# Optimization experiments

Measured on AMD Instinct MI355X. Metric: run time of the kernel, lower is better.

## Reference

```python
import math
import jax, jax.numpy as jnp
import numpy as np

HID_DIM = 1024
N_HEAD = 16
HEAD_DIM = HID_DIM // N_HEAD
NEG_FILL = -1e9


def _alibi_slopes(n_head: int) -> np.ndarray:
    """ALiBi per-head slopes (Press et al. 2021), matching get_slopes()."""
    main = 2 ** int(math.log2(n_head))
    m = (2.0 ** (-8.0 / main)) ** np.arange(1, 1 + main)
    if main < n_head:
        intra = (2.0 ** (-4.0 / main)) ** np.arange(1, 1 + 2 * (n_head - main), 2)
        m = np.concatenate([m, intra])
    return m.astype(np.float32)  # [H]


def setup_inputs() -> dict:
    key = jax.random.key(0)
    k1, k2, k3 = jax.random.split(key, 3)
    B, S = 2, 2048
    x = jax.random.normal(k1, (B, S, HID_DIM), dtype=jnp.float32)
    mask = jnp.ones((B, S), dtype=jnp.int32)
    Wqkv = jax.random.normal(k2, (HID_DIM, 3 * HID_DIM), dtype=jnp.float32) * 0.02
    Wout = jax.random.normal(k3, (HID_DIM, HID_DIM), dtype=jnp.float32) * 0.02
    return {"x": x, "mask": mask, "Wqkv": Wqkv, "Wout": Wout}


def reference(x, mask, Wqkv, Wout):
    B, S, _ = x.shape
    qkv = x @ Wqkv  # [B,S,3*hid]
    q, k, v = jnp.split(qkv, 3, axis=-1)
    k_cache, v_cache = k, v  # current_cache (pre-reshape, [B,S,hid])

    def to_heads(t):
        return t.reshape(B, S, N_HEAD, HEAD_DIM).transpose(0, 2, 1, 3)  # [B,H,S,Dh]

    q, k, v = to_heads(q), to_heads(k), to_heads(v)

    # NOTE: original code computes self.dk but never scales QK^T by it.
    scores = jnp.einsum('bhqd,bhkd->bhqk', q, k)  # [B,H,S,S]

    # ALiBi bias: tril(j - i), zero on/above diagonal elsewhere per torch.tril
    pos = jnp.arange(S)
    alibi = jnp.tril(pos[None, :] - pos[:, None]).astype(scores.dtype)  # [S,S]
    slopes = jnp.asarray(_alibi_slopes(N_HEAD))  # [H]
    scores = scores + slopes[None, :, None, None] * alibi[None, None]

    # padding mask broadcast over key dim: mask[:,None,None,:]
    scores = jnp.where(mask[:, None, None, :] == 0, NEG_FILL, scores)

    probs = jax.nn.softmax(scores, axis=-1)
    attn = jnp.einsum('bhqk,bhkd->bhqd', probs, v)  # [B,H,S,Dh]
    attn = attn.transpose(0, 2, 1, 3).reshape(B, S, HID_DIM)
    out = attn @ Wout  # dropout is identity in eval / p=0
    return out, k_cache, v_cache
```

## Files before the change

### kernel.cpp

```cpp
#include <hip/hip_runtime.h>
#include <hip/hip_bf16.h>
#include <cstdint>
#include <cstddef>

#define HID 1024
#define NH 16
#define DH 64
#define SEQ 2048
#define BATCH 2
#define BS (BATCH*SEQ)
#define LOG2E 1.4426950408889634f
#define PAD 68

typedef __attribute__((ext_vector_type(8))) short bf16x8;
typedef __attribute__((ext_vector_type(4))) float f32x4;

static __device__ __forceinline__ float fast_exp2(float x) {
    return __builtin_amdgcn_exp2f(x);
}

static __device__ __forceinline__ short f2bf(float f) {
    union { __hip_bfloat16 h; short s; } cv;
    cv.h = __float2bfloat16(f);
    return cv.s;
}
static __device__ __forceinline__ unsigned pack2(float a, float b) {
    union { __hip_bfloat162 h2; unsigned u; } cv;
    cv.h2 = __float22bfloat162_rn(make_float2(a, b));
    return cv.u;
}

typedef const __attribute__((address_space(1))) unsigned gas_u32;
typedef __attribute__((address_space(3))) unsigned las_u32;
static __device__ __forceinline__ void gload_lds16(const short* g, short* l) {
    __builtin_amdgcn_global_load_lds((gas_u32*)g, (las_u32*)l, 16, 0, 0);
}

__global__ __launch_bounds__(256)
void prep(const float* __restrict__ Wqkv, const float* __restrict__ Wout,
          const float* __restrict__ x,
          short* __restrict__ wqkvT, short* __restrict__ woutT,
          short* __restrict__ xb)
{
    __shared__ short tl[64][66];
    const int bid = blockIdx.x;
    const int t = threadIdx.x;

    if (bid >= 1024) {
        const float4* x4 = (const float4*)x;
        uint2* xo = (uint2*)xb;
        const int base = (bid - 1024) * 4096 + t;
        #pragma unroll
        for (int i = 0; i < 16; ++i) {
            float4 f = x4[base + i*256];
            xo[base + i*256] = make_uint2(pack2(f.x, f.y), pack2(f.z, f.w));
        }
        return;
    }

    const float* W; short* WT; int Nw, K, k0, n0;
    if (bid < 768) {
        W = Wqkv; WT = wqkvT; Nw = 3072; K = 1024;
        n0 = (bid % 48) * 64; k0 = (bid / 48) * 64;
    } else {
        W = Wout; WT = woutT; Nw = 1024; K = 1024;
        int b2 = bid - 768;
        n0 = (b2 & 15) * 64; k0 = (b2 >> 4) * 64;
    }
    const int r = t >> 2, c0 = (t & 3) * 16;
    const float* src = W + (size_t)(k0 + r) * Nw + n0 + c0;
    #pragma unroll
    for (int i = 0; i < 16; i += 4) {
        float4 f = *(const float4*)(src + i);
        tl[r][c0+i+0] = f2bf(f.x); tl[r][c0+i+1] = f2bf(f.y);
        tl[r][c0+i+2] = f2bf(f.z); tl[r][c0+i+3] = f2bf(f.w);
    }
    __syncthreads();
    short* dst = WT + (size_t)(n0 + r) * K + k0 + c0;
    unsigned buf[8];
    #pragma unroll
    for (int i = 0; i < 8; ++i) {
        unsigned lo = (unsigned short)tl[c0 + 2*i    ][r];
        unsigned hi = (unsigned short)tl[c0 + 2*i + 1][r];
        buf[i] = lo | (hi << 16);
    }
    *(uint4*)dst       = *(uint4*)&buf[0];
    *((uint4*)dst + 1) = *(uint4*)&buf[4];
}

template<int CMODE, int BN>
__global__ __launch_bounds__(256, 3)
void gemm_lds(const short* __restrict__ A, const short* __restrict__ Bt,
              float* __restrict__ Cf,
              float* __restrict__ kc, float* __restrict__ vc,
              short* __restrict__ qb, short* __restrict__ kb, short* __restrict__ vt,
              int M, int N, int K)
{
    constexpr int WN = BN / 2;
    constexpr int NF = WN / 16;
    __shared__ short As[128*64];
    __shared__ short Bs[BN*64];
    const int t    = threadIdx.x;
    const int wave = t >> 6, lane = t & 63;
    const int quad = lane >> 4, l16 = lane & 15;
    const int wrow = (wave & 1) * 64, wcol = (wave >> 1) * WN;
    const int n0 = blockIdx.x * BN, m0 = blockIdx.y * 128;

    f32x4 acc[4][NF];
    #pragma unroll
    for (int mi = 0; mi < 4; ++mi)
        #pragma unroll
        for (int nj = 0; nj < NF; ++nj) acc[mi][nj] = (f32x4){0.f,0.f,0.f,0.f};

    const int lr = lane >> 3;
    const int lc = (lane & 7) * 8;
    const short* Ab = A  + (size_t)(m0 + wave*32       + lr) * K + lc;
    const short* Bb = Bt + (size_t)(n0 + wave*(BN/4)   + lr) * K + lc;
    short* AsW = As + (wave*32)      * 64;
    short* BsW = Bs + (wave*(BN/4))  * 64;

    for (int kt = 0; kt < K; kt += 64) {
        #pragma unroll
        for (int i = 0; i < 4; ++i)
            gload_lds16(Ab + (size_t)(i*8)*K + kt, AsW + i*512);
        #pragma unroll
        for (int i = 0; i < BN/32; ++i)
            gload_lds16(Bb + (size_t)(i*8)*K + kt, BsW + i*512);
        __syncthreads();

        #pragma unroll
        for (int ks = 0; ks < 2; ++ks) {
            bf16x8 af[4], bfr[NF];
            #pragma unroll
            for (int mi = 0; mi < 4; ++mi)
                af[mi] = *(const bf16x8*)&As[(wrow + mi*16 + l16)*64 + ks*32 + quad*8];
            #pragma unroll
            for (int nj = 0; nj < NF; ++nj)
                bfr[nj] = *(const bf16x8*)&Bs[(wcol + nj*16 + l16)*64 + ks*32 + quad*8];
            #pragma unroll
            for (int mi = 0; mi < 4; ++mi)
                #pragma unroll
                for (int nj = 0; nj < NF; ++nj)
                    acc[mi][nj] = __builtin_amdgcn_mfma_f32_16x16x32_bf16(
                        af[mi], bfr[nj], acc[mi][nj], 0, 0, 0);
        }
        __syncthreads();
    }

    const int region = (CMODE == 0) ? (n0 >> 10) : 0;
    #pragma unroll
    for (int mi = 0; mi < 4; ++mi) {
        int rbase = m0 + wrow + mi*16 + quad*4;
        #pragma unroll
        for (int nj = 0; nj < NF; ++nj) {
            int col = n0 + wcol + nj*16 + l16;
            if (CMODE == 1) {
                #pragma unroll
                for (int reg = 0; reg < 4; ++reg)
                    Cf[(size_t)(rbase + reg) * N + col] = acc[mi][nj][reg];
            } else {
                int c = col & 1023;
                if (region == 0) {
                    #pragma unroll
                    for (int reg = 0; reg < 4; ++reg)
                        qb[(size_t)(rbase + reg) * HID + c] = f2bf(acc[mi][nj][reg] * LOG2E);
                } else if (region == 1) {
                    #pragma unroll
                    for (int reg = 0; reg < 4; ++reg) {
                        float v = acc[mi][nj][reg];
                        kc[(size_t)(rbase + reg) * HID + c] = v;
                        if (kb) kb[(size_t)(rbase + reg) * HID + c] = f2bf(v);
                    }
                } else {
                    #pragma unroll
                    for (int reg = 0; reg < 4; ++reg)
                        vc[(size_t)(rbase + reg) * HID + c] = acc[mi][nj][reg];
                    if (vt) {
                        int b = rbase >> 11, s = rbase & 2047;
                        int h = c >> 6, d = c & 63;
                        unsigned u[2] = {pack2(acc[mi][nj][0], acc[mi][nj][1]),
                                         pack2(acc[mi][nj][2], acc[mi][nj][3])};
                        *(uint2*)&vt[((size_t)((b*16 + h)*64 + d)) * SEQ + s] = *(uint2*)u;
                    }
                }
            }
        }
    }
}

template<bool KVB>
__global__ __launch_bounds__(256, 4)
void attn_kernel(const short* qb,
                 const short* __restrict__ kb, const short* __restrict__ vtg,
                 const float* __restrict__ kc, const float* __restrict__ vc,
                 const int*   __restrict__ mask,
                 short* attn_b)
{
    __shared__ short Ks[64*PAD];
    __shared__ short Vs[64*PAD];
    __shared__ short Ps[64*PAD];
    __shared__ float Mk[64];

    const int t    = threadIdx.x;
    const int wave = t >> 6, lane = t & 63;
    const int quad = lane >> 4, l16 = lane & 15;

    const int blk = blockIdx.x;
    const int qt  = blk & 31;
    const int h   = (blk >> 5) & 15;
    const int b   = blk >> 9;
    const int q0  = qt * 64;
    const float slope2 = exp2f(-0.5f * (float)(h + 1)) * LOG2E;
    const int* mb = mask + b * SEQ;

    const int r  = t >> 2;
    const int c0 = (t & 3) * 16;

    const int qrow0 = q0 + 16*wave + quad*4;

    bf16x8 aq[2];
    #pragma unroll
    for (int ks = 0; ks < 2; ++ks)
        aq[ks] = *(const bf16x8*)(qb + ((size_t)(b*SEQ + q0 + 16*wave + l16)) * HID
                                     + h*DH + ks*32 + quad*8);

    float ls[4];
    f32x4 Oacc[4];
    #pragma unroll
    for (int i = 0; i < 4; ++i) {
        ls[i] = 0.f;
        Oacc[i] = (f32x4){0.f,0.f,0.f,0.f};
    }

    if (KVB) {
        uint4 kr0, kr1, vr0, vr1; float mval = 0.f;
        const short* kbase = kb  + ((size_t)(b*SEQ + r)) * HID + h*DH + c0;
        const short* vbase = vtg + ((size_t)((b*NH + h)*DH + r)) * SEQ + c0;

        kr0 = *(const uint4*)(kbase);
        kr1 = *(const uint4*)(kbase + 8);
        vr0 = *(const uint4*)(vbase);
        vr1 = *(const uint4*)(vbase + 8);
        if (t < 64) mval = (mb[t] == 0) ? -2.0e9f : 0.f;

        for (int kt = 0; kt < 32; ++kt) {
            const int j0 = kt * 64;
            __syncthreads();

            *(uint4*)&Ks[r*PAD + c0]     = kr0;
            *(uint4*)&Ks[r*PAD + c0 + 8] = kr1;
            *(uint4*)&Vs[r*PAD + c0]     = vr0;
            *(uint4*)&Vs[r*PAD + c0 + 8] = vr1;
            if (t < 64) Mk[t] = mval;

            if (kt < 31) {
                const short* kn = kbase + (size_t)(j0 + 64) * HID;
                const short* vn = vbase + (j0 + 64);
                kr0 = *(const uint4*)(kn);
                kr1 = *(const uint4*)(kn + 8);
                vr0 = *(const uint4*)(vn);
                vr1 = *(const uint4*)(vn + 8);
                if (t < 64) mval = (mb[j0 + 64 + t] == 0) ? -2.0e9f : 0.f;
            }
            __syncthreads();

            f32x4 S[4];
            #pragma unroll
            for (int nt = 0; nt < 4; ++nt) S[nt] = (f32x4){0.f,0.f,0.f,0.f};
            #pragma unroll
            for (int ks = 0; ks < 2; ++ks) {
                bf16x8 bk[4];
                #pragma unroll
                for (int nt = 0; nt < 4; ++nt)
                    bk[nt] = *(const bf16x8*)&Ks[(nt*16 + l16)*PAD + ks*32 + quad*8];
                __builtin_amdgcn_s_setprio(1);
                #pragma unroll
                for (int nt = 0; nt < 4; ++nt)
                    S[nt] = __builtin_amdgcn_mfma_f32_16x16x32_bf16(
                        aq[ks], bk[nt], S[nt], 0, 0, 0);
                __builtin_amdgcn_s_setprio(0);
            }

            #pragma unroll
            for (int nt = 0; nt < 4; ++nt) {
                int j = j0 + nt*16 + l16;
                float mn  = Mk[nt*16 + l16];
                float fdb = (float)(j - qrow0);
                float p[4];
                #pragma unroll
                for (int reg = 0; reg < 4; ++reg) {
                    float d = fminf(fdb - (float)reg, 0.f);
                    p[reg] = fast_exp2(fmaf(slope2, d, S[nt][reg]) + mn);
                    ls[reg] += p[reg];
                }
                #pragma unroll
                for (int reg = 0; reg < 4; ++reg)
                    Ps[(16*wave + quad*4 + reg)*PAD + nt*16 + l16] = f2bf(p[reg]);
            }

            #pragma unroll
            for (int ks = 0; ks < 2; ++ks) {
                bf16x8 ap = *(const bf16x8*)&Ps[(16*wave + l16)*PAD + ks*32 + quad*8];
                bf16x8 bv[4];
                #pragma unroll
                for (int nt = 0; nt < 4; ++nt)
                    bv[nt] = *(const bf16x8*)&Vs[(nt*16 + l16)*PAD + ks*32 + quad*8];
                __builtin_amdgcn_s_setprio(1);
                #pragma unroll
                for (int nt = 0; nt < 4; ++nt)
                    Oacc[nt] = __builtin_amdgcn_mfma_f32_16x16x32_bf16(
                        ap, bv[nt], Oacc[nt], 0, 0, 0);
                __builtin_amdgcn_s_setprio(0);
            }
        }
    } else {
        for (int kt = 0; kt < 32; ++kt) {
            const int j0 = kt * 64;
            __syncthreads();
            {
                const float* src = kc + ((size_t)(b*SEQ + j0 + r)) * HID + h*DH + c0;
                #pragma unroll
                for (int i = 0; i < 16; i += 4) {
                    float4 f = *(const float4*)(src + i);
                    *(unsigned*)&Ks[r*PAD + c0 + i]     = pack2(f.x, f.y);
                    *(unsigned*)&Ks[r*PAD + c0 + i + 2] = pack2(f.z, f.w);
                }
                int kp = t & 31, db = t >> 5;
                const float* v0 = vc + ((size_t)(b*SEQ + j0 + 2*kp)) * HID + h*DH + db*8;
                const float* v1 = v0 + HID;
                float4 a0 = *(const float4*)v0, a1 = *(const float4*)(v0 + 4);
                float4 b0 = *(const float4*)v1, b1 = *(const float4*)(v1 + 4);
                float va[8]  = {a0.x,a0.y,a0.z,a0.w,a1.x,a1.y,a1.z,a1.w};
                float vb2[8] = {b0.x,b0.y,b0.z,b0.w,b1.x,b1.y,b1.z,b1.w};
                #pragma unroll
                for (int i = 0; i < 8; ++i)
                    *(unsigned*)&Vs[(db*8 + i)*PAD + 2*kp] = pack2(va[i], vb2[i]);
                if (t < 64) Mk[t] = (mb[j0 + t] == 0) ? -2.0e9f : 0.f;
            }
            __syncthreads();

            f32x4 S[4];
            #pragma unroll
            for (int nt = 0; nt < 4; ++nt) S[nt] = (f32x4){0.f,0.f,0.f,0.f};
            #pragma unroll
            for (int ks = 0; ks < 2; ++ks) {
                bf16x8 bk[4];
                #pragma unroll
                for (int nt = 0; nt < 4; ++nt)
                    bk[nt] = *(const bf16x8*)&Ks[(nt*16 + l16)*PAD + ks*32 + quad*8];
                __builtin_amdgcn_s_setprio(1);
                #pragma unroll
                for (int nt = 0; nt < 4; ++nt)
                    S[nt] = __builtin_amdgcn_mfma_f32_16x16x32_bf16(
                        aq[ks], bk[nt], S[nt], 0, 0, 0);
                __builtin_amdgcn_s_setprio(0);
            }

            #pragma unroll
            for (int nt = 0; nt < 4; ++nt) {
                int j = j0 + nt*16 + l16;
                float mn  = Mk[nt*16 + l16];
                float fdb = (float)(j - qrow0);
                float p[4];
                #pragma unroll
                for (int reg = 0; reg < 4; ++reg) {
                    float d = fminf(fdb - (float)reg, 0.f);
                    p[reg] = fast_exp2(fmaf(slope2, d, S[nt][reg]) + mn);
                    ls[reg] += p[reg];
                }
                #pragma unroll
                for (int reg = 0; reg < 4; ++reg)
                    Ps[(16*wave + quad*4 + reg)*PAD + nt*16 + l16] = f2bf(p[reg]);
            }

            #pragma unroll
            for (int ks = 0; ks < 2; ++ks) {
                bf16x8 ap = *(const bf16x8*)&Ps[(16*wave + l16)*PAD + ks*32 + quad*8];
                bf16x8 bv[4];
                #pragma unroll
                for (int nt = 0; nt < 4; ++nt)
                    bv[nt] = *(const bf16x8*)&Vs[(nt*16 + l16)*PAD + ks*32 + quad*8];
                __builtin_amdgcn_s_setprio(1);
                #pragma unroll
                for (int nt = 0; nt < 4; ++nt)
                    Oacc[nt] = __builtin_amdgcn_mfma_f32_16x16x32_bf16(
                        ap, bv[nt], Oacc[nt], 0, 0, 0);
                __builtin_amdgcn_s_setprio(0);
            }
        }
    }

    float rinv[4];
    #pragma unroll
    for (int reg = 0; reg < 4; ++reg) {
        float s0 = ls[reg];
        #pragma unroll
        for (int off = 1; off <= 8; off <<= 1) s0 += __shfl_xor(s0, off, 64);
        rinv[reg] = 1.0f / s0;
    }

    short* ap = attn_b + (size_t)b * SEQ * HID + h * DH;
    #pragma unroll
    for (int nt = 0; nt < 4; ++nt) {
        int dcol = nt*16 + l16;
        #pragma unroll
        for (int reg = 0; reg < 4; ++reg) {
            int row = q0 + 16*wave + quad*4 + reg;
            ap[(size_t)row * HID + dcol] = f2bf(Oacc[nt][reg] * rinv[reg]);
        }
    }
}

extern "C" void kernel_launch(void* const* d_in, const int* in_sizes, int n_in,
                              void* d_out, int out_size, void* d_ws, size_t ws_size,
                              hipStream_t stream)
{
    const float* x    = (const float*)d_in[0];
    const int*   mask = (const int*)  d_in[1];
    const float* Wqkv = (const float*)d_in[2];
    const float* Wout = (const float*)d_in[3];

    float* out = (float*)d_out;
    float* kc  = out + (size_t)BS * HID;
    float* vc  = kc  + (size_t)BS * HID;

    char*  ws    = (char*)d_ws;
    short* qb    = (short*)ws;
    short* wqkvT = (short*)(ws + (8u << 20));
    short* woutT = (short*)(ws + (14u << 20));
    const bool full = ws_size >= (32u << 20);
    short* kb = full ? (short*)(ws + (16u << 20)) : nullptr;
    short* vt = full ? (short*)(ws + (24u << 20)) : nullptr;

    short* xb = (short*)out;

    prep<<<dim3(1280), dim3(256), 0, stream>>>(Wqkv, Wout, x, wqkvT, woutT, xb);

    gemm_lds<0,128><<<dim3(24, 32), dim3(256), 0, stream>>>(
        xb, wqkvT, nullptr, kc, vc, qb, kb, vt, BS, 3*HID, HID);

    if (full)
        attn_kernel<true><<<dim3(1024), dim3(256), 0, stream>>>(
            qb, kb, vt, kc, vc, mask, qb);
    else
        attn_kernel<false><<<dim3(1024), dim3(256), 0, stream>>>(
            qb, nullptr, nullptr, kc, vc, mask, qb);

    gemm_lds<1,64><<<dim3(16, 32), dim3(256), 0, stream>>>(
        qb, woutT, out, nullptr, nullptr, nullptr, nullptr, nullptr, BS, HID, HID);
}
```

Baseline: 225.1 us.

## Enlarge attention tiles to 128 queries and 128 keys with 512-thread blocks

```diff
diff --git a/kernel.cpp b/kernel.cpp
--- a/kernel.cpp
+++ b/kernel.cpp
@@ -10,7 +10,10 @@
 #define BATCH 2
 #define BS (BATCH*SEQ)
 #define LOG2E 1.4426950408889634f
-#define PAD 68
+#define PADK 68
+#define PADV 132
+#define KVBLK 128
+#define QBLK 128
 
 typedef __attribute__((ext_vector_type(8))) short bf16x8;
 typedef __attribute__((ext_vector_type(4))) float f32x4;
@@ -189,32 +192,29 @@
 }
 
 template<bool KVB>
-__global__ __launch_bounds__(256, 4)
+__global__ __launch_bounds__(512, 4)
 void attn_kernel(const short* qb,
                  const short* __restrict__ kb, const short* __restrict__ vtg,
                  const float* __restrict__ kc, const float* __restrict__ vc,
                  const int*   __restrict__ mask,
                  short* attn_b)
 {
-    __shared__ short Ks[64*PAD];
-    __shared__ short Vs[64*PAD];
-    __shared__ short Ps[64*PAD];
-    __shared__ float Mk[64];
+    __shared__ short Ks[KVBLK*PADK];
+    __shared__ short Vs[DH*PADV];
+    __shared__ short Ps[QBLK*PADV];
+    __shared__ float Mk[KVBLK];
 
     const int t    = threadIdx.x;
     const int wave = t >> 6, lane = t & 63;
     const int quad = lane >> 4, l16 = lane & 15;
 
     const int blk = blockIdx.x;
-    const int qt  = blk & 31;
-    const int h   = (blk >> 5) & 15;
-    const int b   = blk >> 9;
-    const int q0  = qt * 64;
+    const int qt  = blk & 15;
+    const int h   = (blk >> 4) & 15;
+    const int b   = blk >> 8;
+    const int q0  = qt * QBLK;
     const float slope2 = exp2f(-0.5f * (float)(h + 1)) * LOG2E;
     const int* mb = mask + b * SEQ;
-
-    const int r  = t >> 2;
-    const int c0 = (t & 3) * 16;
 
     const int qrow0 = q0 + 16*wave + quad*4;
 
@@ -233,56 +233,61 @@
     }
 
     if (KVB) {
+        const int rk = t >> 2;
+        const int ck = (t & 3) * 16;
+        const int rv = t >> 3;
+        const int cv = (t & 7) * 16;
+
         uint4 kr0, kr1, vr0, vr1; float mval = 0.f;
-        const short* kbase = kb  + ((size_t)(b*SEQ + r)) * HID + h*DH + c0;
-        const short* vbase = vtg + ((size_t)((b*NH + h)*DH + r)) * SEQ + c0;
+        const short* kbase = kb  + ((size_t)(b*SEQ + rk)) * HID + h*DH + ck;
+        const short* vbase = vtg + ((size_t)((b*NH + h)*DH + rv)) * SEQ + cv;
 
         kr0 = *(const uint4*)(kbase);
         kr1 = *(const uint4*)(kbase + 8);
         vr0 = *(const uint4*)(vbase);
         vr1 = *(const uint4*)(vbase + 8);
-        if (t < 64) mval = (mb[t] == 0) ? -2.0e9f : 0.f;
-
-        for (int kt = 0; kt < 32; ++kt) {
-            const int j0 = kt * 64;
+        if (t < KVBLK) mval = (mb[t] == 0) ? -2.0e9f : 0.f;
+
+        for (int kt = 0; kt < SEQ/KVBLK; ++kt) {
+            const int j0 = kt * KVBLK;
             __syncthreads();
 
-            *(uint4*)&Ks[r*PAD + c0]     = kr0;
-            *(uint4*)&Ks[r*PAD + c0 + 8] = kr1;
-            *(uint4*)&Vs[r*PAD + c0]     = vr0;
-            *(uint4*)&Vs[r*PAD + c0 + 8] = vr1;
-            if (t < 64) Mk[t] = mval;
-
-            if (kt < 31) {
-                const short* kn = kbase + (size_t)(j0 + 64) * HID;
-                const short* vn = vbase + (j0 + 64);
+            *(uint4*)&Ks[rk*PADK + ck]     = kr0;
+            *(uint4*)&Ks[rk*PADK + ck + 8] = kr1;
+            *(uint4*)&Vs[rv*PADV + cv]     = vr0;
+            *(uint4*)&Vs[rv*PADV + cv + 8] = vr1;
+            if (t < KVBLK) Mk[t] = mval;
+
+            if (kt < SEQ/KVBLK - 1) {
+                const short* kn = kbase + (size_t)(j0 + KVBLK) * HID;
+                const short* vn = vbase + (j0 + KVBLK);
                 kr0 = *(const uint4*)(kn);
                 kr1 = *(const uint4*)(kn + 8);
                 vr0 = *(const uint4*)(vn);
                 vr1 = *(const uint4*)(vn + 8);
-                if (t < 64) mval = (mb[j0 + 64 + t] == 0) ? -2.0e9f : 0.f;
+                if (t < KVBLK) mval = (mb[j0 + KVBLK + t] == 0) ? -2.0e9f : 0.f;
             }
             __syncthreads();
 
-            f32x4 S[4];
-            #pragma unroll
-            for (int nt = 0; nt < 4; ++nt) S[nt] = (f32x4){0.f,0.f,0.f,0.f};
+            f32x4 S[8];
+            #pragma unroll
+            for (int nt = 0; nt < 8; ++nt) S[nt] = (f32x4){0.f,0.f,0.f,0.f};
             #pragma unroll
             for (int ks = 0; ks < 2; ++ks) {
-                bf16x8 bk[4];
-                #pragma unroll
-                for (int nt = 0; nt < 4; ++nt)
-                    bk[nt] = *(const bf16x8*)&Ks[(nt*16 + l16)*PAD + ks*32 + quad*8];
+                bf16x8 bk[8];
+                #pragma unroll
+                for (int nt = 0; nt < 8; ++nt)
+                    bk[nt] = *(const bf16x8*)&Ks[(nt*16 + l16)*PADK + ks*32 + quad*8];
                 __builtin_amdgcn_s_setprio(1);
                 #pragma unroll
-                for (int nt = 0; nt < 4; ++nt)
+                for (int nt = 0; nt < 8; ++nt)
                     S[nt] = __builtin_amdgcn_mfma_f32_16x16x32_bf16(
                         aq[ks], bk[nt], S[nt], 0, 0, 0);
                 __builtin_amdgcn_s_setprio(0);
             }
 
             #pragma unroll
-            for (int nt = 0; nt < 4; ++nt) {
+            for (int nt = 0; nt < 8; ++nt) {
                 int j = j0 + nt*16 + l16;
                 float mn  = Mk[nt*16 + l16];
                 float fdb = (float)(j - qrow0);
@@ -295,16 +300,16 @@
                 }
                 #pragma unroll
                 for (int reg = 0; reg < 4; ++reg)
-                    Ps[(16*wave + quad*4 + reg)*PAD + nt*16 + l16] = f2bf(p[reg]);
-            }
-
-            #pragma unroll
-            for (int ks = 0; ks < 2; ++ks) {
-                bf16x8 ap = *(const bf16x8*)&Ps[(16*wave + l16)*PAD + ks*32 + quad*8];
+                    Ps[(16*wave + quad*4 + reg)*PADV + nt*16 + l16] = f2bf(p[reg]);
+            }
+
+            #pragma unroll
+            for (int ks = 0; ks < 4; ++ks) {
+                bf16x8 ap = *(const bf16x8*)&Ps[(16*wave + l16)*PADV + ks*32 + quad*8];
                 bf16x8 bv[4];
                 #pragma unroll
                 for (int nt = 0; nt < 4; ++nt)
-                    bv[nt] = *(const bf16x8*)&Vs[(nt*16 + l16)*PAD + ks*32 + quad*8];
+                    bv[nt] = *(const bf16x8*)&Vs[(nt*16 + l16)*PADV + ks*32 + quad*8];
                 __builtin_amdgcn_s_setprio(1);
                 #pragma unroll
                 for (int nt = 0; nt < 4; ++nt)
@@ -314,18 +319,20 @@
             }
         }
     } else {
-        for (int kt = 0; kt < 32; ++kt) {
-            const int j0 = kt * 64;
+        const int rk = t >> 2;
+        const int ck = (t & 3) * 16;
+        for (int kt = 0; kt < SEQ/KVBLK; ++kt) {
+            const int j0 = kt * KVBLK;
             __syncthreads();
             {
-                const float* src = kc + ((size_t)(b*SEQ + j0 + r)) * HID + h*DH + c0;
+                const float* src = kc + ((size_t)(b*SEQ + j0 + rk)) * HID + h*DH + ck;
                 #pragma unroll
                 for (int i = 0; i < 16; i += 4) {
                     float4 f = *(const float4*)(src + i);
-                    *(unsigned*)&Ks[r*PAD + c0 + i]     = pack2(f.x, f.y);
-                    *(unsigned*)&Ks[r*PAD + c0 + i + 2] = pack2(f.z, f.w);
+                    *(unsigned*)&Ks[rk*PADK + ck + i]     = pack2(f.x, f.y);
+                    *(unsigned*)&Ks[rk*PADK + ck + i + 2] = pack2(f.z, f.w);
                 }
-                int kp = t & 31, db = t >> 5;
+                int kp = t & 63, db = t >> 6;
                 const float* v0 = vc + ((size_t)(b*SEQ + j0 + 2*kp)) * HID + h*DH + db*8;
                 const float* v1 = v0 + HID;
                 float4 a0 = *(const float4*)v0, a1 = *(const float4*)(v0 + 4);
@@ -334,30 +341,30 @@
                 float vb2[8] = {b0.x,b0.y,b0.z,b0.w,b1.x,b1.y,b1.z,b1.w};
                 #pragma unroll
                 for (int i = 0; i < 8; ++i)
-                    *(unsigned*)&Vs[(db*8 + i)*PAD + 2*kp] = pack2(va[i], vb2[i]);
-                if (t < 64) Mk[t] = (mb[j0 + t] == 0) ? -2.0e9f : 0.f;
+                    *(unsigned*)&Vs[(db*8 + i)*PADV + 2*kp] = pack2(va[i], vb2[i]);
+                if (t < KVBLK) Mk[t] = (mb[j0 + t] == 0) ? -2.0e9f : 0.f;
             }
             __syncthreads();
 
-            f32x4 S[4];
-            #pragma unroll
-            for (int nt = 0; nt < 4; ++nt) S[nt] = (f32x4){0.f,0.f,0.f,0.f};
+            f32x4 S[8];
+            #pragma unroll
+            for (int nt = 0; nt < 8; ++nt) S[nt] = (f32x4){0.f,0.f,0.f,0.f};
             #pragma unroll
             for (int ks = 0; ks < 2; ++ks) {
-                bf16x8 bk[4];
-                #pragma unroll
-                for (int nt = 0; nt < 4; ++nt)
-                    bk[nt] = *(const bf16x8*)&Ks[(nt*16 + l16)*PAD + ks*32 + quad*8];
+                bf16x8 bk[8];
+                #pragma unroll
+                for (int nt = 0; nt < 8; ++nt)
+                    bk[nt] = *(const bf16x8*)&Ks[(nt*16 + l16)*PADK + ks*32 + quad*8];
                 __builtin_amdgcn_s_setprio(1);
                 #pragma unroll
-                for (int nt = 0; nt < 4; ++nt)
+                for (int nt = 0; nt < 8; ++nt)
                     S[nt] = __builtin_amdgcn_mfma_f32_16x16x32_bf16(
                         aq[ks], bk[nt], S[nt], 0, 0, 0);
                 __builtin_amdgcn_s_setprio(0);
             }
 
             #pragma unroll
-            for (int nt = 0; nt < 4; ++nt) {
+            for (int nt = 0; nt < 8; ++nt) {
                 int j = j0 + nt*16 + l16;
                 float mn  = Mk[nt*16 + l16];
                 float fdb = (float)(j - qrow0);
@@ -370,16 +377,16 @@
                 }
                 #pragma unroll
                 for (int reg = 0; reg < 4; ++reg)
-                    Ps[(16*wave + quad*4 + reg)*PAD + nt*16 + l16] = f2bf(p[reg]);
-            }
-
-            #pragma unroll
-            for (int ks = 0; ks < 2; ++ks) {
-                bf16x8 ap = *(const bf16x8*)&Ps[(16*wave + l16)*PAD + ks*32 + quad*8];
+                    Ps[(16*wave + quad*4 + reg)*PADV + nt*16 + l16] = f2bf(p[reg]);
+            }
+
+            #pragma unroll
+            for (int ks = 0; ks < 4; ++ks) {
+                bf16x8 ap = *(const bf16x8*)&Ps[(16*wave + l16)*PADV + ks*32 + quad*8];
                 bf16x8 bv[4];
                 #pragma unroll
                 for (int nt = 0; nt < 4; ++nt)
-                    bv[nt] = *(const bf16x8*)&Vs[(nt*16 + l16)*PAD + ks*32 + quad*8];
+                    bv[nt] = *(const bf16x8*)&Vs[(nt*16 + l16)*PADV + ks*32 + quad*8];
                 __builtin_amdgcn_s_setprio(1);
                 #pragma unroll
                 for (int nt = 0; nt < 4; ++nt)
@@ -440,10 +447,10 @@
         xb, wqkvT, nullptr, kc, vc, qb, kb, vt, BS, 3*HID, HID);
 
     if (full)
-        attn_kernel<true><<<dim3(1024), dim3(256), 0, stream>>>(
+        attn_kernel<true><<<dim3(512), dim3(512), 0, stream>>>(
             qb, kb, vt, kc, vc, mask, qb);
     else
-        attn_kernel<false><<<dim3(1024), dim3(256), 0, stream>>>(
+        attn_kernel<false><<<dim3(512), dim3(512), 0, stream>>>(
             qb, nullptr, nullptr, kc, vc, mask, qb);
 
     gemm_lds<1,64><<<dim3(16, 32), dim3(256), 0, stream>>>(
```

Measured after the change: 235.1 us. +4.4%, slower.

## Double-buffer K/V shared tiles in attention to drop one barrier per step

Applied to the files above, without the earlier changes.

```diff
diff --git a/kernel.cpp b/kernel.cpp
--- a/kernel.cpp
+++ b/kernel.cpp
@@ -10,7 +10,7 @@
 #define BATCH 2
 #define BS (BATCH*SEQ)
 #define LOG2E 1.4426950408889634f
-#define PAD 68
+#define PADK 68
 
 typedef __attribute__((ext_vector_type(8))) short bf16x8;
 typedef __attribute__((ext_vector_type(4))) float f32x4;
@@ -189,17 +189,17 @@
 }
 
 template<bool KVB>
-__global__ __launch_bounds__(256, 4)
+__global__ __launch_bounds__(256, 3)
 void attn_kernel(const short* qb,
                  const short* __restrict__ kb, const short* __restrict__ vtg,
                  const float* __restrict__ kc, const float* __restrict__ vc,
                  const int*   __restrict__ mask,
                  short* attn_b)
 {
-    __shared__ short Ks[64*PAD];
-    __shared__ short Vs[64*PAD];
-    __shared__ short Ps[64*PAD];
-    __shared__ float Mk[64];
+    __shared__ short Ks[2][64*PADK];
+    __shared__ short Vs[2][64*PADK];
+    __shared__ short Ps[64*PADK];
+    __shared__ float Mk[2][64];
 
     const int t    = threadIdx.x;
     const int wave = t >> 6, lane = t & 63;
@@ -243,15 +243,16 @@
         vr1 = *(const uint4*)(vbase + 8);
         if (t < 64) mval = (mb[t] == 0) ? -2.0e9f : 0.f;
 
+        *(uint4*)&Ks[0][r*PADK + c0]     = kr0;
+        *(uint4*)&Ks[0][r*PADK + c0 + 8] = kr1;
+        *(uint4*)&Vs[0][r*PADK + c0]     = vr0;
+        *(uint4*)&Vs[0][r*PADK + c0 + 8] = vr1;
+        if (t < 64) Mk[0][t] = mval;
+        __syncthreads();
+
         for (int kt = 0; kt < 32; ++kt) {
+            const int cur = kt & 1;
             const int j0 = kt * 64;
-            __syncthreads();
-
-            *(uint4*)&Ks[r*PAD + c0]     = kr0;
-            *(uint4*)&Ks[r*PAD + c0 + 8] = kr1;
-            *(uint4*)&Vs[r*PAD + c0]     = vr0;
-            *(uint4*)&Vs[r*PAD + c0 + 8] = vr1;
-            if (t < 64) Mk[t] = mval;
 
             if (kt < 31) {
                 const short* kn = kbase + (size_t)(j0 + 64) * HID;
@@ -262,7 +263,6 @@
                 vr1 = *(const uint4*)(vn + 8);
                 if (t < 64) mval = (mb[j0 + 64 + t] == 0) ? -2.0e9f : 0.f;
             }
-            __syncthreads();
 
             f32x4 S[4];
             #pragma unroll
@@ -272,7 +272,7 @@
                 bf16x8 bk[4];
                 #pragma unroll
                 for (int nt = 0; nt < 4; ++nt)
-                    bk[nt] = *(const bf16x8*)&Ks[(nt*16 + l16)*PAD + ks*32 + quad*8];
+                    bk[nt] = *(const bf16x8*)&Ks[cur][(nt*16 + l16)*PADK + ks*32 + quad*8];
                 __builtin_amdgcn_s_setprio(1);
                 #pragma unroll
                 for (int nt = 0; nt < 4; ++nt)
@@ -284,7 +284,7 @@
             #pragma unroll
             for (int nt = 0; nt < 4; ++nt) {
                 int j = j0 + nt*16 + l16;
-                float mn  = Mk[nt*16 + l16];
+                float mn  = Mk[cur][nt*16 + l16];
                 float fdb = (float)(j - qrow0);
                 float p[4];
                 #pragma unroll
@@ -295,22 +295,32 @@
                 }
                 #pragma unroll
                 for (int reg = 0; reg < 4; ++reg)
-                    Ps[(16*wave + quad*4 + reg)*PAD + nt*16 + l16] = f2bf(p[reg]);
+                    Ps[(16*wave + quad*4 + reg)*PADK + nt*16 + l16] = f2bf(p[reg]);
             }
 
             #pragma unroll
             for (int ks = 0; ks < 2; ++ks) {
-                bf16x8 ap = *(const bf16x8*)&Ps[(16*wave + l16)*PAD + ks*32 + quad*8];
+                bf16x8 ap = *(const bf16x8*)&Ps[(16*wave + l16)*PADK + ks*32 + quad*8];
                 bf16x8 bv[4];
                 #pragma unroll
                 for (int nt = 0; nt < 4; ++nt)
-                    bv[nt] = *(const bf16x8*)&Vs[(nt*16 + l16)*PAD + ks*32 + quad*8];
+                    bv[nt] = *(const bf16x8*)&Vs[cur][(nt*16 + l16)*PADK + ks*32 + quad*8];
                 __builtin_amdgcn_s_setprio(1);
                 #pragma unroll
                 for (int nt = 0; nt < 4; ++nt)
                     Oacc[nt] = __builtin_amdgcn_mfma_f32_16x16x32_bf16(
                         ap, bv[nt], Oacc[nt], 0, 0, 0);
                 __builtin_amdgcn_s_setprio(0);
+            }
+
+            if (kt < 31) {
+                const int nxt = cur ^ 1;
+                *(uint4*)&Ks[nxt][r*PADK + c0]     = kr0;
+                *(uint4*)&Ks[nxt][r*PADK + c0 + 8] = kr1;
+                *(uint4*)&Vs[nxt][r*PADK + c0]     = vr0;
+                *(uint4*)&Vs[nxt][r*PADK + c0 + 8] = vr1;
+                if (t < 64) Mk[nxt][t] = mval;
+                __syncthreads();
             }
         }
     } else {
@@ -322,8 +332,8 @@
                 #pragma unroll
                 for (int i = 0; i < 16; i += 4) {
                     float4 f = *(const float4*)(src + i);
-                    *(unsigned*)&Ks[r*PAD + c0 + i]     = pack2(f.x, f.y);
-                    *(unsigned*)&Ks[r*PAD + c0 + i + 2] = pack2(f.z, f.w);
+                    *(unsigned*)&Ks[0][r*PADK + c0 + i]     = pack2(f.x, f.y);
+                    *(unsigned*)&Ks[0][r*PADK + c0 + i + 2] = pack2(f.z, f.w);
                 }
                 int kp = t & 31, db = t >> 5;
                 const float* v0 = vc + ((size_t)(b*SEQ + j0 + 2*kp)) * HID + h*DH + db*8;
@@ -334,8 +344,8 @@
                 float vb2[8] = {b0.x,b0.y,b0.z,b0.w,b1.x,b1.y,b1.z,b1.w};
                 #pragma unroll
                 for (int i = 0; i < 8; ++i)
-                    *(unsigned*)&Vs[(db*8 + i)*PAD + 2*kp] = pack2(va[i], vb2[i]);
-                if (t < 64) Mk[t] = (mb[j0 + t] == 0) ? -2.0e9f : 0.f;
+                    *(unsigned*)&Vs[0][(db*8 + i)*PADK + 2*kp] = pack2(va[i], vb2[i]);
+                if (t < 64) Mk[0][t] = (mb[j0 + t] == 0) ? -2.0e9f : 0.f;
             }
             __syncthreads();
 
@@ -347,7 +357,7 @@
                 bf16x8 bk[4];
                 #pragma unroll
                 for (int nt = 0; nt < 4; ++nt)
-                    bk[nt] = *(const bf16x8*)&Ks[(nt*16 + l16)*PAD + ks*32 + quad*8];
+                    bk[nt] = *(const bf16x8*)&Ks[0][(nt*16 + l16)*PADK + ks*32 + quad*8];
                 __builtin_amdgcn_s_setprio(1);
                 #pragma unroll
                 for (int nt = 0; nt < 4; ++nt)
@@ -359,7 +369,7 @@
             #pragma unroll
             for (int nt = 0; nt < 4; ++nt) {
                 int j = j0 + nt*16 + l16;
-                float mn  = Mk[nt*16 + l16];
+                float mn  = Mk[0][nt*16 + l16];
                 float fdb = (float)(j - qrow0);
                 float p[4];
                 #pragma unroll
@@ -370,16 +380,16 @@
                 }
                 #pragma unroll
                 for (int reg = 0; reg < 4; ++reg)
-                    Ps[(16*wave + quad*4 + reg)*PAD + nt*16 + l16] = f2bf(p[reg]);
+                    Ps[(16*wave + quad*4 + reg)*PADK + nt*16 + l16] = f2bf(p[reg]);
             }
 
             #pragma unroll
             for (int ks = 0; ks < 2; ++ks) {
-                bf16x8 ap = *(const bf16x8*)&Ps[(16*wave + l16)*PAD + ks*32 + quad*8];
+                bf16x8 ap = *(const bf16x8*)&Ps[(16*wave + l16)*PADK + ks*32 + quad*8];
                 bf16x8 bv[4];
                 #pragma unroll
                 for (int nt = 0; nt < 4; ++nt)
-                    bv[nt] = *(const bf16x8*)&Vs[(nt*16 + l16)*PAD + ks*32 + quad*8];
+                    bv[nt] = *(const bf16x8*)&Vs[0][(nt*16 + l16)*PADK + ks*32 + quad*8];
                 __builtin_amdgcn_s_setprio(1);
                 #pragma unroll
                 for (int nt = 0; nt < 4; ++nt)
```

Result: slower. 234.4 us (+4.1%).

## Split attention over two key halves with a separate combine kernel

Applied to the files above, without the earlier changes.

```diff
diff --git a/kernel.cpp b/kernel.cpp
--- a/kernel.cpp
+++ b/kernel.cpp
@@ -10,7 +10,7 @@
 #define BATCH 2
 #define BS (BATCH*SEQ)
 #define LOG2E 1.4426950408889634f
-#define PAD 68
+#define PADK 68
 
 typedef __attribute__((ext_vector_type(8))) short bf16x8;
 typedef __attribute__((ext_vector_type(4))) float f32x4;
@@ -28,6 +28,9 @@
     union { __hip_bfloat162 h2; unsigned u; } cv;
     cv.h2 = __float22bfloat162_rn(make_float2(a, b));
     return cv.u;
+}
+static __device__ __forceinline__ float bfu(unsigned short v) {
+    union { float f; unsigned u; } x; x.u = (unsigned)v << 16; return x.f;
 }
 
 typedef const __attribute__((address_space(1))) unsigned gas_u32;
@@ -189,16 +192,18 @@
 }
 
 template<bool KVB>
-__global__ __launch_bounds__(256, 4)
+__global__ __launch_bounds__(256, 6)
 void attn_kernel(const short* qb,
                  const short* __restrict__ kb, const short* __restrict__ vtg,
                  const float* __restrict__ kc, const float* __restrict__ vc,
                  const int*   __restrict__ mask,
-                 short* attn_b)
+                 short* attn_b,
+                 short* __restrict__ opart,
+                 float* __restrict__ lsp)
 {
-    __shared__ short Ks[64*PAD];
-    __shared__ short Vs[64*PAD];
-    __shared__ short Ps[64*PAD];
+    __shared__ short Ks[64*PADK];
+    __shared__ short Vs[64*PADK];
+    __shared__ short Ps[64*PADK];
     __shared__ float Mk[64];
 
     const int t    = threadIdx.x;
@@ -207,9 +212,12 @@
 
     const int blk = blockIdx.x;
     const int qt  = blk & 31;
-    const int h   = (blk >> 5) & 15;
-    const int b   = blk >> 9;
+    int sp, h, b;
+    if (KVB) { sp = (blk >> 5) & 1; h = (blk >> 6) & 15; b = blk >> 10; }
+    else     { sp = 0;              h = (blk >> 5) & 15; b = blk >> 9;  }
     const int q0  = qt * 64;
+    const int j00 = sp << 10;
+    const int NT  = KVB ? 16 : 32;
     const float slope2 = exp2f(-0.5f * (float)(h + 1)) * LOG2E;
     const int* mb = mask + b * SEQ;
 
@@ -234,28 +242,29 @@
 
     if (KVB) {
         uint4 kr0, kr1, vr0, vr1; float mval = 0.f;
-        const short* kbase = kb  + ((size_t)(b*SEQ + r)) * HID + h*DH + c0;
-        const short* vbase = vtg + ((size_t)((b*NH + h)*DH + r)) * SEQ + c0;
+        const short* kbase = kb  + ((size_t)(b*SEQ + j00 + r)) * HID + h*DH + c0;
+        const short* vbase = vtg + ((size_t)((b*NH + h)*DH + r)) * SEQ + j00 + c0;
 
         kr0 = *(const uint4*)(kbase);
         kr1 = *(const uint4*)(kbase + 8);
         vr0 = *(const uint4*)(vbase);
         vr1 = *(const uint4*)(vbase + 8);
-        if (t < 64) mval = (mb[t] == 0) ? -2.0e9f : 0.f;
-
-        for (int kt = 0; kt < 32; ++kt) {
-            const int j0 = kt * 64;
+        mval = (mb[j00 + t & 63 ? j00 + (t & 63) : j00] == 0) ? -2.0e9f : 0.f;
+        mval = (t < 64) ? ((mb[j00 + t] == 0) ? -2.0e9f : 0.f) : 0.f;
+
+        for (int kt = 0; kt < NT; ++kt) {
+            const int j0 = j00 + kt * 64;
             __syncthreads();
 
-            *(uint4*)&Ks[r*PAD + c0]     = kr0;
-            *(uint4*)&Ks[r*PAD + c0 + 8] = kr1;
-            *(uint4*)&Vs[r*PAD + c0]     = vr0;
-            *(uint4*)&Vs[r*PAD + c0 + 8] = vr1;
+            *(uint4*)&Ks[r*PADK + c0]     = kr0;
+            *(uint4*)&Ks[r*PADK + c0 + 8] = kr1;
+            *(uint4*)&Vs[r*PADK + c0]     = vr0;
+            *(uint4*)&Vs[r*PADK + c0 + 8] = vr1;
             if (t < 64) Mk[t] = mval;
 
-            if (kt < 31) {
-                const short* kn = kbase + (size_t)(j0 + 64) * HID;
-                const short* vn = vbase + (j0 + 64);
+            if (kt < NT - 1) {
+                const short* kn = kbase + (size_t)((kt + 1) * 64) * HID;
+                const short* vn = vbase + (kt + 1) * 64;
                 kr0 = *(const uint4*)(kn);
                 kr1 = *(const uint4*)(kn + 8);
                 vr0 = *(const uint4*)(vn);
@@ -272,7 +281,7 @@
                 bf16x8 bk[4];
                 #pragma unroll
                 for (int nt = 0; nt < 4; ++nt)
-                    bk[nt] = *(const bf16x8*)&Ks[(nt*16 + l16)*PAD + ks*32 + quad*8];
+                    bk[nt] = *(const bf16x8*)&Ks[(nt*16 + l16)*PADK + ks*32 + quad*8];
                 __builtin_amdgcn_s_setprio(1);
                 #pragma unroll
                 for (int nt = 0; nt < 4; ++nt)
@@ -295,22 +304,45 @@
                 }
                 #pragma unroll
                 for (int reg = 0; reg < 4; ++reg)
-                    Ps[(16*wave + quad*4 + reg)*PAD + nt*16 + l16] = f2bf(p[reg]);
+                    Ps[(16*wave + quad*4 + reg)*PADK + nt*16 + l16] = f2bf(p[reg]);
             }
 
             #pragma unroll
             for (int ks = 0; ks < 2; ++ks) {
-                bf16x8 ap = *(const bf16x8*)&Ps[(16*wave + l16)*PAD + ks*32 + quad*8];
+                bf16x8 ap = *(const bf16x8*)&Ps[(16*wave + l16)*PADK + ks*32 + quad*8];
                 bf16x8 bv[4];
                 #pragma unroll
                 for (int nt = 0; nt < 4; ++nt)
-                    bv[nt] = *(const bf16x8*)&Vs[(nt*16 + l16)*PAD + ks*32 + quad*8];
+                    bv[nt] = *(const bf16x8*)&Vs[(nt*16 + l16)*PADK + ks*32 + quad*8];
                 __builtin_amdgcn_s_setprio(1);
                 #pragma unroll
                 for (int nt = 0; nt < 4; ++nt)
                     Oacc[nt] = __builtin_amdgcn_mfma_f32_16x16x32_bf16(
                         ap, bv[nt], Oacc[nt], 0, 0, 0);
                 __builtin_amdgcn_s_setprio(0);
+            }
+        }
+
+        float s4[4];
+        #pragma unroll
+        for (int reg = 0; reg < 4; ++reg) {
+            float s0 = ls[reg];
+            #pragma unroll
+            for (int off = 1; off <= 8; off <<= 1) s0 += __shfl_xor(s0, off, 64);
+            s4[reg] = s0;
+        }
+        if (l16 == 0) {
+            float4 v = make_float4(s4[0], s4[1], s4[2], s4[3]);
+            *(float4*)&lsp[(((size_t)(b*NH + h)) * 2 + sp) * SEQ + qrow0] = v;
+        }
+        short* po = opart + (size_t)sp * BS * HID + (size_t)b * SEQ * HID + h * DH;
+        #pragma unroll
+        for (int nt = 0; nt < 4; ++nt) {
+            int dcol = nt*16 + l16;
+            #pragma unroll
+            for (int reg = 0; reg < 4; ++reg) {
+                int row = q0 + 16*wave + quad*4 + reg;
+                po[(size_t)row * HID + dcol] = f2bf(Oacc[nt][reg]);
             }
         }
     } else {
@@ -322,8 +354,8 @@
                 #pragma unroll
                 for (int i = 0; i < 16; i += 4) {
                     float4 f = *(const float4*)(src + i);
-                    *(unsigned*)&Ks[r*PAD + c0 + i]     = pack2(f.x, f.y);
-                    *(unsigned*)&Ks[r*PAD + c0 + i + 2] = pack2(f.z, f.w);
+                    *(unsigned*)&Ks[r*PADK + c0 + i]     = pack2(f.x, f.y);
+                    *(unsigned*)&Ks[r*PADK + c0 + i + 2] = pack2(f.z, f.w);
                 }
                 int kp = t & 31, db = t >> 5;
                 const float* v0 = vc + ((size_t)(b*SEQ + j0 + 2*kp)) * HID + h*DH + db*8;
@@ -334,7 +366,7 @@
                 float vb2[8] = {b0.x,b0.y,b0.z,b0.w,b1.x,b1.y,b1.z,b1.w};
                 #pragma unroll
                 for (int i = 0; i < 8; ++i)
-                    *(unsigned*)&Vs[(db*8 + i)*PAD + 2*kp] = pack2(va[i], vb2[i]);
+                    *(unsigned*)&Vs[(db*8 + i)*PADK + 2*kp] = pack2(va[i], vb2[i]);
                 if (t < 64) Mk[t] = (mb[j0 + t] == 0) ? -2.0e9f : 0.f;
             }
             __syncthreads();
@@ -347,13 +379,11 @@
                 bf16x8 bk[4];
                 #pragma unroll
                 for (int nt = 0; nt < 4; ++nt)
-                    bk[nt] = *(const bf16x8*)&Ks[(nt*16 + l16)*PAD + ks*32 + quad*8];
-                __builtin_amdgcn_s_setprio(1);
+                    bk[nt] = *(const bf16x8*)&Ks[(nt*16 + l16)*PADK + ks*32 + quad*8];
                 #pragma unroll
                 for (int nt = 0; nt < 4; ++nt)
                     S[nt] = __builtin_amdgcn_mfma_f32_16x16x32_bf16(
                         aq[ks], bk[nt], S[nt], 0, 0, 0);
-                __builtin_amdgcn_s_setprio(0);
             }
 
             #pragma unroll
@@ -370,45 +400,69 @@
                 }
                 #pragma unroll
                 for (int reg = 0; reg < 4; ++reg)
-                    Ps[(16*wave + quad*4 + reg)*PAD + nt*16 + l16] = f2bf(p[reg]);
+                    Ps[(16*wave + quad*4 + reg)*PADK + nt*16 + l16] = f2bf(p[reg]);
             }
 
             #pragma unroll
             for (int ks = 0; ks < 2; ++ks) {
-                bf16x8 ap = *(const bf16x8*)&Ps[(16*wave + l16)*PAD + ks*32 + quad*8];
+                bf16x8 ap = *(const bf16x8*)&Ps[(16*wave + l16)*PADK + ks*32 + quad*8];
                 bf16x8 bv[4];
                 #pragma unroll
                 for (int nt = 0; nt < 4; ++nt)
-                    bv[nt] = *(const bf16x8*)&Vs[(nt*16 + l16)*PAD + ks*32 + quad*8];
-                __builtin_amdgcn_s_setprio(1);
+                    bv[nt] = *(const bf16x8*)&Vs[(nt*16 + l16)*PADK + ks*32 + quad*8];
                 #pragma unroll
                 for (int nt = 0; nt < 4; ++nt)
                     Oacc[nt] = __builtin_amdgcn_mfma_f32_16x16x32_bf16(
                         ap, bv[nt], Oacc[nt], 0, 0, 0);
-                __builtin_amdgcn_s_setprio(0);
-            }
-        }
-    }
-
-    float rinv[4];
-    #pragma unroll
-    for (int reg = 0; reg < 4; ++reg) {
-        float s0 = ls[reg];
-        #pragma unroll
-        for (int off = 1; off <= 8; off <<= 1) s0 += __shfl_xor(s0, off, 64);
-        rinv[reg] = 1.0f / s0;
-    }
-
-    short* ap = attn_b + (size_t)b * SEQ * HID + h * DH;
-    #pragma unroll
-    for (int nt = 0; nt < 4; ++nt) {
-        int dcol = nt*16 + l16;
+            }
+        }
+
+        float rinv[4];
         #pragma unroll
         for (int reg = 0; reg < 4; ++reg) {
-            int row = q0 + 16*wave + quad*4 + reg;
-            ap[(size_t)row * HID + dcol] = f2bf(Oacc[nt][reg] * rinv[reg]);
-        }
-    }
+            float s0 = ls[reg];
+            #pragma unroll
+            for (int off = 1; off <= 8; off <<= 1) s0 += __shfl_xor(s0, off, 64);
+            rinv[reg] = 1.0f / s0;
+        }
+        short* ap = attn_b + (size_t)b * SEQ * HID + h * DH;
+        #pragma unroll
+        for (int nt = 0; nt < 4; ++nt) {
+            int dcol = nt*16 + l16;
+            #pragma unroll
+            for (int reg = 0; reg < 4; ++reg) {
+                int row = q0 + 16*wave + quad*4 + reg;
+                ap[(size_t)row * HID + dcol] = f2bf(Oacc[nt][reg] * rinv[reg]);
+            }
+        }
+    }
+}
+
+__global__ __launch_bounds__(256)
+void combine(const short* __restrict__ op, const float* __restrict__ lsp,
+             short* __restrict__ qb)
+{
+    const int i = blockIdx.x * 256 + threadIdx.x;
+    const size_t off = (size_t)i * 8;
+    const int row = (int)(off >> 10);
+    const int col = (int)(off & 1023);
+    const int b = row >> 11, s = row & 2047, h = col >> 6;
+    const float* lb = lsp + ((size_t)(b*NH + h)) * 2 * SEQ;
+    const float inv = 1.0f / (lb[s] + lb[SEQ + s]);
+    uint4 a = *(const uint4*)(op + off);
+    uint4 c = *(const uint4*)(op + (size_t)BS * HID + off);
+    unsigned ua[4] = {a.x, a.y, a.z, a.w};
+    unsigned uc[4] = {c.x, c.y, c.z, c.w};
+    unsigned uo[4];
+    #pragma unroll
+    for (int k = 0; k < 4; ++k) {
+        float a0 = bfu((unsigned short)(ua[k] & 0xFFFF));
+        float a1 = bfu((unsigned short)(ua[k] >> 16));
+        float c0 = bfu((unsigned short)(uc[k] & 0xFFFF));
+        float c1 = bfu((unsigned short)(uc[k] >> 16));
+        uo[k] = pack2((a0 + c0) * inv, (a1 + c1) * inv);
+    }
+    *(uint4*)(qb + off) = *(uint4*)uo;
 }
 
 extern "C" void kernel_launch(void* const* d_in, const int* in_sizes, int n_in,
@@ -432,19 +486,23 @@
     short* kb = full ? (short*)(ws + (16u << 20)) : nullptr;
     short* vt = full ? (short*)(ws + (24u << 20)) : nullptr;
 
-    short* xb = (short*)out;
+    short* xb    = (short*)out;
+    short* opart = (short*)out;
+    float* lsp   = (float*)wqkvT;
 
     prep<<<dim3(1280), dim3(256), 0, stream>>>(Wqkv, Wout, x, wqkvT, woutT, xb);
 
     gemm_lds<0,128><<<dim3(24, 32), dim3(256), 0, stream>>>(
         xb, wqkvT, nullptr, kc, vc, qb, kb, vt, BS, 3*HID, HID);
 
-    if (full)
-        attn_kernel<true><<<dim3(1024), dim3(256), 0, stream>>>(
-            qb, kb, vt, kc, vc, mask, qb);
-    else
+    if (full) {
+        attn_kernel<true><<<dim3(2048), dim3(256), 0, stream>>>(
+            qb, kb, vt, kc, vc, mask, qb, opart, lsp);
+        combine<<<dim3(BS*HID/8/256), dim3(256), 0, stream>>>(opart, lsp, qb);
+    } else {
         attn_kernel<false><<<dim3(1024), dim3(256), 0, stream>>>(
-            qb, nullptr, nullptr, kc, vc, mask, qb);
+            qb, nullptr, nullptr, kc, vc, mask, qb, nullptr, nullptr);
+    }
 
     gemm_lds<1,64><<<dim3(16, 32), dim3(256), 0, stream>>>(
         qb, woutT, out, nullptr, nullptr, nullptr, nullptr, nullptr, BS, HID, HID);
```

Measured after the change: 411.8 us. 1.83x slower.
